# Kernel optimization log

Measured on AMD Instinct MI355X. Metric: run time of the kernel, lower is better.

Reference implementation:

```python
import jax, jax.numpy as jnp
import numpy as np

HID = 1024
NH = 4  # heads for GAT conv1 and all attention blocks
FF = 2048
SLOPE = 0.2


def _ln(x, g, b):
    m = x.mean(-1, keepdims=True)
    v = ((x - m) ** 2).mean(-1, keepdims=True)
    return (x - m) / jnp.sqrt(v + 1e-5) * g + b


def _mha(q, k, v, in_w, in_b, out_w, out_b, nh):
    # q:[B,Lq,E], k/v:[B,Lk,E]; torch MultiheadAttention math (eval mode)
    B, Lq, E = q.shape
    hd = E // nh
    wq, wk, wv = jnp.split(in_w, 3, axis=0)
    bq, bk, bv = jnp.split(in_b, 3)
    qh = (q @ wq.T + bq).reshape(B, Lq, nh, hd)
    kh = (k @ wk.T + bk).reshape(B, -1, nh, hd)
    vh = (v @ wv.T + bv).reshape(B, -1, nh, hd)
    s = jnp.einsum('bqhd,bkhd->bhqk', qh, kh) / jnp.sqrt(jnp.asarray(hd, q.dtype))
    a = jax.nn.softmax(s, axis=-1)
    o = jnp.einsum('bhqk,bkhd->bqhd', a, vh).reshape(B, Lq, E)
    return o @ out_w.T + out_b


def _gatv2(x, edge_index, w_l, b_l, w_r, b_r, att, bias, heads, out_ch):
    # PyG GATv2Conv, flow='target_to_source': i (aggregation dst) = edge_index[0], j = edge_index[1]
    n = x.shape[0]
    dst = edge_index[0]
    src = edge_index[1]
    x_l = (x @ w_l + b_l).reshape(n, heads, out_ch)
    x_r = (x @ w_r + b_r).reshape(n, heads, out_ch)
    msg = x_l[src]                                   # [E,H,C] gathered source features
    e = jax.nn.leaky_relu(msg + x_r[dst], SLOPE)     # [E,H,C]
    alpha = (e * att).sum(-1)                        # [E,H]
    amax = jax.ops.segment_max(alpha, dst, num_segments=n)
    alpha = jnp.exp(alpha - amax[dst])
    denom = jax.ops.segment_sum(alpha, dst, num_segments=n)
    alpha = alpha / (denom[dst] + 1e-16)
    out = jax.ops.segment_sum(msg * alpha[..., None], dst, num_segments=n)
    return out.reshape(n, heads * out_ch) + bias


def setup_inputs() -> dict:
    key = jax.random.key(0)
    ks = iter(jax.random.split(key, 64))
    N, DF, B, L, E_rand = 8000, 768, 32, 14, 96000
    w = lambda *s: jax.random.normal(next(ks), s, jnp.float32) * 0.02
    z = lambda *s: jnp.zeros(s, jnp.float32)
    o = lambda *s: jnp.ones(s, jnp.float32)
    ei = jax.random.randint(next(ks), (2, E_rand), 0, N, jnp.int32)
    self_loops = jnp.tile(jnp.arange(N, dtype=jnp.int32)[None, :], (2, 1))
    inp = {
        'img_feat': jax.random.normal(next(ks), (B, HID), jnp.float32),
        'node_features': jax.random.normal(next(ks), (N, DF), jnp.float32),
        'edge_index': jnp.concatenate([ei, self_loops], axis=1),
        'target_idx': jax.random.randint(next(ks), (L,), 0, N, jnp.int32),
        # GATv2 conv1: 768 -> 4 heads x 256
        'gat1_wl': w(DF, HID), 'gat1_bl': z(HID), 'gat1_wr': w(DF, HID), 'gat1_br': z(HID),
        'gat1_att': w(NH, HID // NH), 'gat1_bias': z(HID),
        # GATv2 conv2: 1024 -> 1 head x 1024
        'gat2_wl': w(HID, HID), 'gat2_bl': z(HID), 'gat2_wr': w(HID, HID), 'gat2_br': z(HID),
        'gat2_att': w(1, HID), 'gat2_bias': z(HID),
        # cross-modal MHA + FFN layer
        'xa_in_w': w(3 * HID, HID), 'xa_in_b': z(3 * HID), 'xa_out_w': w(HID, HID), 'xa_out_b': z(HID),
        'xl_l1_w': w(FF, HID), 'xl_l1_b': z(FF), 'xl_l2_w': w(HID, FF), 'xl_l2_b': z(HID),
        'xl_n1_g': o(HID), 'xl_n1_b': z(HID), 'xl_n2_g': o(HID), 'xl_n2_b': z(HID),
        # 2-layer TransformerEncoder (stacked leading dim = layer)
        'enc_in_w': w(2, 3 * HID, HID), 'enc_in_b': z(2, 3 * HID),
        'enc_out_w': w(2, HID, HID), 'enc_out_b': z(2, HID),
        'enc_l1_w': w(2, FF, HID), 'enc_l1_b': z(2, FF),
        'enc_l2_w': w(2, HID, FF), 'enc_l2_b': z(2, HID),
        'enc_n1_g': o(2, HID), 'enc_n1_b': z(2, HID),
        'enc_n2_g': o(2, HID), 'enc_n2_b': z(2, HID),
        'cls_w': w(1, HID), 'cls_b': z(1),
    }
    return inp


def reference(img_feat, node_features, edge_index, target_idx,
              gat1_wl, gat1_bl, gat1_wr, gat1_br, gat1_att, gat1_bias,
              gat2_wl, gat2_bl, gat2_wr, gat2_br, gat2_att, gat2_bias,
              xa_in_w, xa_in_b, xa_out_w, xa_out_b,
              xl_l1_w, xl_l1_b, xl_l2_w, xl_l2_b, xl_n1_g, xl_n1_b, xl_n2_g, xl_n2_b,
              enc_in_w, enc_in_b, enc_out_w, enc_out_b, enc_l1_w, enc_l1_b, enc_l2_w, enc_l2_b,
              enc_n1_g, enc_n1_b, enc_n2_g, enc_n2_b, cls_w, cls_b):
    x = _gatv2(node_features, edge_index, gat1_wl, gat1_bl, gat1_wr, gat1_br, gat1_att, gat1_bias, NH, HID // NH)
    x = jax.nn.leaky_relu(x, SLOPE)
    x = _gatv2(x, edge_index, gat2_wl, gat2_bl, gat2_wr, gat2_br, gat2_att, gat2_bias, 1, HID)
    t = x[target_idx]                                  # [L, HID]
    B = img_feat.shape[0]
    L = t.shape[0]
    q = jnp.broadcast_to(t[None], (B, L, HID))
    kv = img_feat[:, None, :]                          # [B, 1, HID]
    attn = _mha(q, kv, kv, xa_in_w, xa_in_b, xa_out_w, xa_out_b, NH)
    src = _ln(t[None] + attn, xl_n1_g, xl_n1_b)
    ff = jax.nn.relu(src @ xl_l1_w.T + xl_l1_b) @ xl_l2_w.T + xl_l2_b
    src = _ln(src + ff, xl_n2_g, xl_n2_b)
    for i in range(2):  # TransformerEncoder, post-norm, relu, eval mode
        a = _mha(src, src, src, enc_in_w[i], enc_in_b[i], enc_out_w[i], enc_out_b[i], NH)
        src = _ln(src + a, enc_n1_g[i], enc_n1_b[i])
        f = jax.nn.relu(src @ enc_l1_w[i].T + enc_l1_b[i]) @ enc_l2_w[i].T + enc_l2_b[i]
        src = _ln(src + f, enc_n2_g[i], enc_n2_b[i])
    return (src @ cls_w.T + cls_b)[..., 0]             # [B, L]
```

## Files before the change

### kernel.cpp

```cpp
#include <hip/hip_runtime.h>
#include <hip/hip_bf16.h>

typedef __bf16 bf16;
typedef bf16 bf16x8 __attribute__((ext_vector_type(8)));
typedef bf16 bf16x4 __attribute__((ext_vector_type(4)));
typedef float f32x4 __attribute__((ext_vector_type(4)));

#define HID 1024
#define FFD 2048
#define DEGCAP 1024

typedef __attribute__((address_space(3))) void lds_void;
typedef const __attribute__((address_space(1))) void gm_void;

__device__ __forceinline__ void gload_lds16(const bf16* g, bf16* l)
{
    __builtin_amdgcn_global_load_lds((gm_void*)g, (lds_void*)l, 16, 0, 0);
}

__global__ __launch_bounds__(256) void cvt_bf16_kernel(
    const float* __restrict__ src, bf16* __restrict__ dst, long n)
{
    long i = ((long)blockIdx.x * 256 + threadIdx.x) * 4;
    if (i >= n) return;
    float4 f = *(const float4*)&src[i];
    bf16x4 v = {(bf16)f.x, (bf16)f.y, (bf16)f.z, (bf16)f.w};
    *(bf16x4*)&dst[i] = v;
}

__global__ __launch_bounds__(256) void cvt_t_bf16_kernel(
    const float* __restrict__ in, bf16* __restrict__ out, int R, int C)
{
    __shared__ bf16 tile[32][33];
    const int c0 = blockIdx.x * 32, r0 = blockIdx.y * 32;
    const int tx = threadIdx.x & 31, ty = threadIdx.x >> 5;
#pragma unroll
    for (int i = ty; i < 32; i += 8)
        tile[i][tx] = (bf16)in[(long)(r0 + i) * C + c0 + tx];
    __syncthreads();
#pragma unroll
    for (int i = ty; i < 32; i += 8)
        out[(long)(c0 + i) * R + r0 + tx] = tile[tx][i];
}

template <int ACT, int OUTBF16>
__global__ __launch_bounds__(256) void gemm_bf16_kernel(
    const bf16* __restrict__ A, const bf16* __restrict__ B,
    const float* __restrict__ bias, void* __restrict__ Cp,
    int M, int N, int K)
{
    const int tid  = threadIdx.x;
    const int bn   = blockIdx.x, bm = blockIdx.y;
    const int lane = tid & 63, wave = tid >> 6;
    const int wr   = wave >> 1, wc = wave & 1;

    __shared__ bf16 As[128][32];
    __shared__ bf16 Bs[128][32];

    f32x4 acc[4][4] = {};

    const int srow = wave * 16 + (lane >> 2);
    const int scol = (lane & 3) << 3;
    const long ga0 = (long)min(bm * 128 + srow,      M - 1) * K + scol;
    const long ga1 = (long)min(bm * 128 + srow + 64, M - 1) * K + scol;
    const long gb0 = (long)(bn * 128 + srow)      * K + scol;
    const long gb1 = (long)(bn * 128 + srow + 64) * K + scol;
    bf16* ldsA0 = &As[0][0] + wave * 512;
    bf16* ldsA1 = &As[0][0] + 2048 + wave * 512;
    bf16* ldsB0 = &Bs[0][0] + wave * 512;
    bf16* ldsB1 = &Bs[0][0] + 2048 + wave * 512;

    const int quad = lane >> 4;
    const int mr   = lane & 15;
    const int kf   = quad * 8;

    for (int k0 = 0; k0 < K; k0 += 32) {
        gload_lds16(A + ga0 + k0, ldsA0);
        gload_lds16(A + ga1 + k0, ldsA1);
        gload_lds16(B + gb0 + k0, ldsB0);
        gload_lds16(B + gb1 + k0, ldsB1);
        __syncthreads();

        bf16x8 af[4], bfr[4];
#pragma unroll
        for (int i = 0; i < 4; ++i) af[i]  = *(const bf16x8*)&As[wr * 64 + i * 16 + mr][kf];
#pragma unroll
        for (int j = 0; j < 4; ++j) bfr[j] = *(const bf16x8*)&Bs[wc * 64 + j * 16 + mr][kf];
#pragma unroll
        for (int i = 0; i < 4; ++i)
#pragma unroll
            for (int j = 0; j < 4; ++j)
                acc[i][j] = __builtin_amdgcn_mfma_f32_16x16x32_bf16(af[i], bfr[j], acc[i][j], 0, 0, 0);
        __syncthreads();
    }

    const int crow = quad * 4;
#pragma unroll
    for (int i = 0; i < 4; ++i) {
#pragma unroll
        for (int j = 0; j < 4; ++j) {
            const int   col = bn * 128 + wc * 64 + j * 16 + mr;
            const float bv  = bias[col];
#pragma unroll
            for (int r = 0; r < 4; ++r) {
                const int row = bm * 128 + wr * 64 + i * 16 + crow + r;
                if (row < M) {
                    float v = acc[i][j][r] + bv;
                    if (ACT == 1) v = fmaxf(v, 0.f);
                    if (OUTBF16) ((bf16*)Cp)[(long)row * N + col] = (bf16)v;
                    else         ((float*)Cp)[(long)row * N + col] = v;
                }
            }
        }
    }
}

template <int KS>
__global__ __launch_bounds__(256) void gemm_sk_kernel(
    const float* __restrict__ A, const float* __restrict__ Bt,
    float* __restrict__ part, int M, int N, int K)
{
    const int tid  = threadIdx.x;
    const int bn   = blockIdx.x, bm = blockIdx.y, kz = blockIdx.z;
    const int lane = tid & 63, wave = tid >> 6;
    const int wr   = wave >> 1, wc = wave & 1;

    __shared__ bf16 As[128][40];
    __shared__ bf16 Bs[128][40];

    f32x4 acc[4][4] = {};

    const int  lr = tid >> 2;
    const int  lc = (tid & 3) << 3;
    const long a0 = (long)min(bm * 128 + lr,      M - 1) * K;
    const long a1 = (long)min(bm * 128 + lr + 64, M - 1) * K;
    const long b0 = (long)(bn * 128 + lr)      * K;
    const long b1 = (long)(bn * 128 + lr + 64) * K;

    const int quad = lane >> 4;
    const int mr   = lane & 15;
    const int kf   = quad * 8;

    const int Kc   = K / KS;
    const int kbeg = kz * Kc, kend = kbeg + Kc;

    float4 ra[4], rb[4];
    auto load_chunk = [&](int k0) {
        ra[0] = *(const float4*)&A[a0 + k0 + lc];
        ra[1] = *(const float4*)&A[a0 + k0 + lc + 4];
        ra[2] = *(const float4*)&A[a1 + k0 + lc];
        ra[3] = *(const float4*)&A[a1 + k0 + lc + 4];
        rb[0] = *(const float4*)&Bt[b0 + k0 + lc];
        rb[1] = *(const float4*)&Bt[b0 + k0 + lc + 4];
        rb[2] = *(const float4*)&Bt[b1 + k0 + lc];
        rb[3] = *(const float4*)&Bt[b1 + k0 + lc + 4];
    };

    load_chunk(kbeg);
    for (int k0 = kbeg; k0 < kend; k0 += 32) {
        {
            bf16x8 v0 = {(bf16)ra[0].x,(bf16)ra[0].y,(bf16)ra[0].z,(bf16)ra[0].w,
                         (bf16)ra[1].x,(bf16)ra[1].y,(bf16)ra[1].z,(bf16)ra[1].w};
            *(bf16x8*)&As[lr][lc] = v0;
            bf16x8 v1 = {(bf16)ra[2].x,(bf16)ra[2].y,(bf16)ra[2].z,(bf16)ra[2].w,
                         (bf16)ra[3].x,(bf16)ra[3].y,(bf16)ra[3].z,(bf16)ra[3].w};
            *(bf16x8*)&As[lr + 64][lc] = v1;
            bf16x8 v2 = {(bf16)rb[0].x,(bf16)rb[0].y,(bf16)rb[0].z,(bf16)rb[0].w,
                         (bf16)rb[1].x,(bf16)rb[1].y,(bf16)rb[1].z,(bf16)rb[1].w};
            *(bf16x8*)&Bs[lr][lc] = v2;
            bf16x8 v3 = {(bf16)rb[2].x,(bf16)rb[2].y,(bf16)rb[2].z,(bf16)rb[2].w,
                         (bf16)rb[3].x,(bf16)rb[3].y,(bf16)rb[3].z,(bf16)rb[3].w};
            *(bf16x8*)&Bs[lr + 64][lc] = v3;
        }
        __syncthreads();
        if (k0 + 32 < kend) load_chunk(k0 + 32);

        bf16x8 af[4], bfr[4];
#pragma unroll
        for (int i = 0; i < 4; ++i) af[i]  = *(const bf16x8*)&As[wr * 64 + i * 16 + mr][kf];
#pragma unroll
        for (int j = 0; j < 4; ++j) bfr[j] = *(const bf16x8*)&Bs[wc * 64 + j * 16 + mr][kf];
#pragma unroll
        for (int i = 0; i < 4; ++i)
#pragma unroll
            for (int j = 0; j < 4; ++j)
                acc[i][j] = __builtin_amdgcn_mfma_f32_16x16x32_bf16(af[i], bfr[j], acc[i][j], 0, 0, 0);
        __syncthreads();
    }

    const int crow = quad * 4;
    float* dst = part + (size_t)kz * M * N;
#pragma unroll
    for (int i = 0; i < 4; ++i) {
#pragma unroll
        for (int j = 0; j < 4; ++j) {
            const int col = bn * 128 + wc * 64 + j * 16 + mr;
#pragma unroll
            for (int r = 0; r < 4; ++r) {
                const int row = bm * 128 + wr * 64 + i * 16 + crow + r;
                if (row < M) dst[(long)row * N + col] = acc[i][j][r];
            }
        }
    }
}

template <int ACT, int KS>
__global__ __launch_bounds__(256) void sk_reduce_kernel(
    const float* __restrict__ part, const float* __restrict__ bias,
    float* __restrict__ C, long MN, int N)
{
    long i = ((long)blockIdx.x * 256 + threadIdx.x) * 4;
    if (i >= MN) return;
    float4 s = *(const float4*)&part[i];
#pragma unroll
    for (int k = 1; k < KS; ++k) {
        float4 p = *(const float4*)&part[(size_t)k * MN + i];
        s.x += p.x; s.y += p.y; s.z += p.z; s.w += p.w;
    }
    const int col = (int)(i % N);
    float4 bv = *(const float4*)&bias[col];
    s.x += bv.x; s.y += bv.y; s.z += bv.z; s.w += bv.w;
    if (ACT) {
        s.x = fmaxf(s.x, 0.f); s.y = fmaxf(s.y, 0.f);
        s.z = fmaxf(s.z, 0.f); s.w = fmaxf(s.w, 0.f);
    }
    *(float4*)&C[i] = s;
}

__global__ void zero_i32_kernel(int* __restrict__ p, int n)
{
    int i = blockIdx.x * 256 + threadIdx.x;
    if (i < n) p[i] = 0;
}

__global__ void hist_kernel(const int* __restrict__ ei, int E, int* __restrict__ deg)
{
    int e = blockIdx.x * 256 + threadIdx.x;
    if (e < E) atomicAdd(&deg[ei[e]], 1);
}

__global__ void scan_kernel(const int* __restrict__ deg, int* __restrict__ rowstart,
                            int* __restrict__ cursor, int n)
{
    __shared__ int sm[1024];
    __shared__ int carry;
    if (threadIdx.x == 0) carry = 0;
    __syncthreads();
    for (int base = 0; base < n; base += 1024) {
        int i = base + threadIdx.x;
        int v = (i < n) ? deg[i] : 0;
        sm[threadIdx.x] = v;
        __syncthreads();
        for (int off = 1; off < 1024; off <<= 1) {
            int t = (threadIdx.x >= off) ? sm[threadIdx.x - off] : 0;
            __syncthreads();
            sm[threadIdx.x] += t;
            __syncthreads();
        }
        if (i < n) { int ex = carry + sm[threadIdx.x] - v; rowstart[i] = ex; cursor[i] = ex; }
        __syncthreads();
        if (threadIdx.x == 0) carry += sm[1023];
        __syncthreads();
    }
    if (threadIdx.x == 0) rowstart[n] = carry;
}

__global__ void scatter_kernel(const int* __restrict__ ei, int E,
                               int* __restrict__ cursor, int* __restrict__ eidx)
{
    int e = blockIdx.x * 256 + threadIdx.x;
    if (e < E) { int p = atomicAdd(&cursor[ei[e]], 1); eidx[p] = e; }
}

template <int NH, int LRELU, int OUTBF16>
__global__ __launch_bounds__(256) void gat_fused_kernel(
    const bf16* __restrict__ xl, const bf16* __restrict__ xr,
    const float* __restrict__ att,
    const int* __restrict__ ei, const int* __restrict__ rowstart,
    const int* __restrict__ eidx, const float* __restrict__ bias,
    void* __restrict__ outp, int E)
{
    const int n = blockIdx.x;
    const int tid = threadIdx.x, lane = tid & 63, wave = tid >> 6;
    const int rs = rowstart[n];
    int deg = rowstart[n + 1] - rs;
    if (deg > DEGCAP) deg = DEGCAP;

    __shared__ bf16  xr_sm[HID];
    __shared__ int   src_sm[DEGCAP];
    __shared__ float alpha_sm[DEGCAP * NH];

    {
        const int c0 = tid * 4;
        *(bf16x4*)&xr_sm[c0] = *(const bf16x4*)&xr[(long)n * HID + c0];
    }
    for (int j = tid; j < deg; j += 256)
        src_sm[j] = ei[E + eidx[rs + j]];
    __syncthreads();

    for (int j = wave; j < deg; j += 4) {
        const int s = src_sm[j];
        const int c0 = lane * 16;
        bf16x8 a0 = *(const bf16x8*)&xl[(long)s * HID + c0];
        bf16x8 a1 = *(const bf16x8*)&xl[(long)s * HID + c0 + 8];
        bf16x8 b0 = *(const bf16x8*)&xr_sm[c0];
        bf16x8 b1 = *(const bf16x8*)&xr_sm[c0 + 8];
        float4 t0 = *(const float4*)&att[c0];
        float4 t1 = *(const float4*)&att[c0 + 4];
        float4 t2 = *(const float4*)&att[c0 + 8];
        float4 t3 = *(const float4*)&att[c0 + 12];
        const float* at = (const float*)&t0;
        float av[16] = {t0.x,t0.y,t0.z,t0.w, t1.x,t1.y,t1.z,t1.w,
                        t2.x,t2.y,t2.z,t2.w, t3.x,t3.y,t3.z,t3.w};
        (void)at;
        float acc = 0.f;
#pragma unroll
        for (int t = 0; t < 8; ++t) {
            float v = (float)a0[t] + (float)b0[t];
            v = v > 0.f ? v : 0.2f * v;
            acc += v * av[t];
            float w = (float)a1[t] + (float)b1[t];
            w = w > 0.f ? w : 0.2f * w;
            acc += w * av[8 + t];
        }
        if (NH == 4) {
#pragma unroll
            for (int o = 1; o < 16; o <<= 1) acc += __shfl_xor(acc, o);
            if ((lane & 15) == 0) alpha_sm[j * NH + (lane >> 4)] = acc;
        } else {
#pragma unroll
            for (int o = 1; o < 64; o <<= 1) acc += __shfl_xor(acc, o);
            if (lane == 0) alpha_sm[j] = acc;
        }
    }
    __syncthreads();

    if (wave < NH) {
        float m = -1e30f;
        for (int j = lane; j < deg; j += 64) m = fmaxf(m, alpha_sm[j * NH + wave]);
        for (int o = 32; o; o >>= 1) m = fmaxf(m, __shfl_down(m, o));
        m = __shfl(m, 0);
        float s = 0.f;
        for (int j = lane; j < deg; j += 64) s += expf(alpha_sm[j * NH + wave] - m);
        for (int o = 32; o; o >>= 1) s += __shfl_down(s, o);
        s = __shfl(s, 0);
        const float dinv = 1.f / (s + 1e-16f);
        for (int j = lane; j < deg; j += 64)
            alpha_sm[j * NH + wave] = expf(alpha_sm[j * NH + wave] - m) * dinv;
    }
    __syncthreads();

    const int c0 = tid * 4;
    const int hh = (NH == 4) ? (tid >> 6) : 0;
    float a0 = 0, a1 = 0, a2 = 0, a3 = 0;
    for (int j = 0; j < deg; ++j) {
        const float alpha = alpha_sm[j * NH + hh];
        bf16x4 mv = *(const bf16x4*)&xl[(long)src_sm[j] * HID + c0];
        a0 += alpha * (float)mv[0]; a1 += alpha * (float)mv[1];
        a2 += alpha * (float)mv[2]; a3 += alpha * (float)mv[3];
    }
    float o4[4] = {a0, a1, a2, a3};
#pragma unroll
    for (int k = 0; k < 4; ++k) {
        float v = o4[k] + bias[c0 + k];
        if (LRELU) v = v > 0.f ? v : 0.2f * v;
        if (OUTBF16) ((bf16*)outp)[(long)n * HID + c0 + k] = (bf16)v;
        else         ((float*)outp)[(long)n * HID + c0 + k] = v;
    }
}

__device__ __forceinline__ void ln_finish(float v[4], int c0, const float* g,
                                          const float* beta, float* outrow)
{
    float s1 = v[0] + v[1] + v[2] + v[3];
    float s2 = v[0] * v[0] + v[1] * v[1] + v[2] * v[2] + v[3] * v[3];
    __shared__ float red[8];
    for (int o = 32; o; o >>= 1) { s1 += __shfl_down(s1, o); s2 += __shfl_down(s2, o); }
    const int wave = threadIdx.x >> 6, lane = threadIdx.x & 63;
    if (lane == 0) { red[wave] = s1; red[4 + wave] = s2; }
    __syncthreads();
    if (threadIdx.x == 0) {
        red[0] += red[1] + red[2] + red[3];
        red[4] += red[5] + red[6] + red[7];
    }
    __syncthreads();
    const float mean = red[0] * (1.f / HID);
    const float var  = fmaxf(red[4] * (1.f / HID) - mean * mean, 0.f);
    const float rstd = rsqrtf(var + 1e-5f);
#pragma unroll
    for (int k = 0; k < 4; ++k) {
        int c = c0 + k;
        outrow[c] = (v[k] - mean) * rstd * g[c] + beta[c];
    }
}

__global__ __launch_bounds__(256) void ln_cross_kernel(
    const float* __restrict__ x2, const int* __restrict__ tidx,
    const float* __restrict__ attnb, const float* __restrict__ g,
    const float* __restrict__ beta, float* __restrict__ out, int L)
{
    const int row = blockIdx.x;
    const int b = row / L, l = row - b * L;
    const long tr = (long)tidx[l] * HID, ar = (long)b * HID;
    const int c0 = threadIdx.x * 4;
    float v[4];
#pragma unroll
    for (int k = 0; k < 4; ++k)
        v[k] = x2[tr + c0 + k] + attnb[ar + c0 + k];
    ln_finish(v, c0, g, beta, out + (long)row * HID);
}

__global__ __launch_bounds__(256) void ln_res_kernel(
    float* __restrict__ srcio, const float* __restrict__ delta,
    const float* __restrict__ g, const float* __restrict__ beta)
{
    const long row = blockIdx.x;
    const int c0 = threadIdx.x * 4;
    float v[4];
#pragma unroll
    for (int k = 0; k < 4; ++k)
        v[k] = srcio[row * HID + c0 + k] + delta[row * HID + c0 + k];
    ln_finish(v, c0, g, beta, srcio + row * HID);
}

__global__ __launch_bounds__(256) void self_attn_kernel(
    const float* __restrict__ qkv, float* __restrict__ out, int L)
{
    const int b = blockIdx.x >> 2, h = blockIdx.x & 3;
    const int tid = threadIdx.x;
    __shared__ float q[16][256], kk[16][256], vv[16][256];
    __shared__ float sc[16][16];
    for (int i = tid; i < L * 256; i += 256) {
        const int l = i >> 8, d = i & 255;
        const long rb = (long)(b * L + l) * 3072 + h * 256 + d;
        q[l][d]  = qkv[rb];
        kk[l][d] = qkv[rb + 1024];
        vv[l][d] = qkv[rb + 2048];
    }
    __syncthreads();
    if (tid < L * L) {
        const int l1 = tid / L, l2 = tid - l1 * L;
        float s = 0.f;
        for (int d = 0; d < 256; ++d) s += q[l1][d] * kk[l2][d];
        sc[l1][l2] = s * 0.0625f;
    }
    __syncthreads();
    if (tid < L) {
        float mx = -1e30f;
        for (int j = 0; j < L; ++j) mx = fmaxf(mx, sc[tid][j]);
        float ssum = 0.f;
        for (int j = 0; j < L; ++j) { float e = expf(sc[tid][j] - mx); sc[tid][j] = e; ssum += e; }
        const float inv = 1.f / ssum;
        for (int j = 0; j < L; ++j) sc[tid][j] *= inv;
    }
    __syncthreads();
    for (int l1 = 0; l1 < L; ++l1) {
        float a = 0.f;
        for (int l2 = 0; l2 < L; ++l2) a += sc[l1][l2] * vv[l2][tid];
        out[(long)(b * L + l1) * HID + h * 256 + tid] = a;
    }
}

__global__ __launch_bounds__(256) void cls_kernel(
    const float* __restrict__ src, const float* __restrict__ w,
    const float* __restrict__ b, float* __restrict__ out, int rows)
{
    const int row = blockIdx.x * 4 + (threadIdx.x >> 6);
    const int lane = threadIdx.x & 63;
    if (row >= rows) return;
    float s = 0.f;
    for (int c = lane; c < HID; c += 64) s += src[(long)row * HID + c] * w[c];
    for (int o = 32; o; o >>= 1) s += __shfl_down(s, o);
    if (lane == 0) out[row] = s + b[0];
}

extern "C" void kernel_launch(void* const* d_in, const int* in_sizes, int n_in,
                              void* d_out, int out_size, void* d_ws, size_t ws_size,
                              hipStream_t stream)
{
    const float* img_feat      = (const float*)d_in[0];
    const float* node_features = (const float*)d_in[1];
    const int*   edge_index    = (const int*)d_in[2];
    const int*   target_idx    = (const int*)d_in[3];
    const float* gat1_wl  = (const float*)d_in[4];
    const float* gat1_bl  = (const float*)d_in[5];
    const float* gat1_wr  = (const float*)d_in[6];
    const float* gat1_br  = (const float*)d_in[7];
    const float* gat1_att = (const float*)d_in[8];
    const float* gat1_bias= (const float*)d_in[9];
    const float* gat2_wl  = (const float*)d_in[10];
    const float* gat2_bl  = (const float*)d_in[11];
    const float* gat2_wr  = (const float*)d_in[12];
    const float* gat2_br  = (const float*)d_in[13];
    const float* gat2_att = (const float*)d_in[14];
    const float* gat2_bias= (const float*)d_in[15];
    const float* xa_in_w  = (const float*)d_in[16];
    const float* xa_in_b  = (const float*)d_in[17];
    const float* xa_out_w = (const float*)d_in[18];
    const float* xa_out_b = (const float*)d_in[19];
    const float* xl_l1_w  = (const float*)d_in[20];
    const float* xl_l1_b  = (const float*)d_in[21];
    const float* xl_l2_w  = (const float*)d_in[22];
    const float* xl_l2_b  = (const float*)d_in[23];
    const float* xl_n1_g  = (const float*)d_in[24];
    const float* xl_n1_b  = (const float*)d_in[25];
    const float* xl_n2_g  = (const float*)d_in[26];
    const float* xl_n2_b  = (const float*)d_in[27];
    const float* enc_in_w = (const float*)d_in[28];
    const float* enc_in_b = (const float*)d_in[29];
    const float* enc_out_w= (const float*)d_in[30];
    const float* enc_out_b= (const float*)d_in[31];
    const float* enc_l1_w = (const float*)d_in[32];
    const float* enc_l1_b = (const float*)d_in[33];
    const float* enc_l2_w = (const float*)d_in[34];
    const float* enc_l2_b = (const float*)d_in[35];
    const float* enc_n1_g = (const float*)d_in[36];
    const float* enc_n1_b = (const float*)d_in[37];
    const float* enc_n2_g = (const float*)d_in[38];
    const float* enc_n2_b = (const float*)d_in[39];
    const float* cls_w    = (const float*)d_in[40];
    const float* cls_b    = (const float*)d_in[41];

    const int DF = in_sizes[4] / HID;
    const int Nn = in_sizes[1] / DF;
    const int E  = in_sizes[2] / 2;
    const int L  = in_sizes[3];
    const int B  = in_sizes[0] / HID;
    const int R  = B * L;

    char* basep = (char*)d_ws;
    size_t off = 0;
    auto alloc = [&](size_t bytes) -> char* {
        char* r = basep + off; off += (bytes + 255) & ~(size_t)255; return r;
    };
    size_t regA_need = 0;
    {
        auto sz = [&](size_t b) { regA_need += (b + 255) & ~(size_t)255; };
        sz((size_t)Nn * DF * 2); sz((size_t)DF * HID * 2); sz((size_t)DF * HID * 2);
        sz((size_t)HID * HID * 2); sz((size_t)HID * HID * 2); sz((size_t)Nn * HID * 2);
    }
    size_t regA_bytes = regA_need > (size_t)Nn * HID * 4 ? regA_need : (size_t)Nn * HID * 4;
    char* regionA = alloc(regA_bytes);
    {
        size_t aoff = 0;
        auto allocA = [&](size_t bytes) -> char* {
            char* r = regionA + aoff; aoff += (bytes + 255) & ~(size_t)255; return r;
        };
        bf16* nfb  = (bf16*)allocA((size_t)Nn * DF * 2);
        bf16* w1lT = (bf16*)allocA((size_t)DF * HID * 2);
        bf16* w1rT = (bf16*)allocA((size_t)DF * HID * 2);
        bf16* w2lT = (bf16*)allocA((size_t)HID * HID * 2);
        bf16* w2rT = (bf16*)allocA((size_t)HID * HID * 2);
        bf16* x1   = (bf16*)allocA((size_t)Nn * HID * 2);

        float* x2  = (float*)regionA;

        bf16* xlb = (bf16*)alloc((size_t)Nn * HID * 2);
        bf16* xrb = (bf16*)alloc((size_t)Nn * HID * 2);
        int*   deg      = (int*)alloc((size_t)Nn * 4);
        int*   rowstart = (int*)alloc((size_t)(Nn + 1) * 4);
        int*   cursor   = (int*)alloc((size_t)(Nn + 1) * 4);
        int*   eidx     = (int*)alloc((size_t)E * 4);
        float* skpart   = (float*)alloc((size_t)4 * R * 3 * HID * 4);

        char* qb = (char*)xlb; size_t qoff = 0;
        auto alloc2 = [&](size_t bytes) -> char* {
            char* r = qb + qoff; qoff += (bytes + 255) & ~(size_t)255; return r;
        };
        float* vproj  = (float*)alloc2((size_t)B * HID * 4);
        float* attnb  = (float*)alloc2((size_t)B * HID * 4);
        float* srcbuf = (float*)alloc2((size_t)R * HID * 4);
        float* h1buf  = (float*)alloc2((size_t)R * FFD * 4);
        float* ffbuf  = (float*)alloc2((size_t)R * HID * 4);
        float* qkvbuf = (float*)alloc2((size_t)R * 3 * HID * 4);
        float* aoutbuf= (float*)alloc2((size_t)R * HID * 4);

        const int gE  = (E + 255) / 256;
        const int gMn = (Nn + 127) / 128;

        auto gemm_sk4 = [&](const float* A, const float* Bt, const float* bias,
                            float* C, int M, int N, int K, int act) {
            gemm_sk_kernel<4><<<dim3(N / 128, (M + 127) / 128, 4), 256, 0, stream>>>(
                A, Bt, skpart, M, N, K);
            long MN = (long)M * N;
            int g = (int)((MN / 4 + 255) / 256);
            if (act) sk_reduce_kernel<1,4><<<g, 256, 0, stream>>>(skpart, bias, C, MN, N);
            else     sk_reduce_kernel<0,4><<<g, 256, 0, stream>>>(skpart, bias, C, MN, N);
        };
        auto gemm_sk8 = [&](const float* A, const float* Bt, const float* bias,
                            float* C, int M, int N, int K, int act) {
            gemm_sk_kernel<8><<<dim3(N / 128, (M + 127) / 128, 8), 256, 0, stream>>>(
                A, Bt, skpart, M, N, K);
            long MN = (long)M * N;
            int g = (int)((MN / 4 + 255) / 256);
            if (act) sk_reduce_kernel<1,8><<<g, 256, 0, stream>>>(skpart, bias, C, MN, N);
            else     sk_reduce_kernel<0,8><<<g, 256, 0, stream>>>(skpart, bias, C, MN, N);
        };

        zero_i32_kernel<<<(Nn + 255) / 256, 256, 0, stream>>>(deg, Nn);
        hist_kernel<<<gE, 256, 0, stream>>>(edge_index, E, deg);
        scan_kernel<<<1, 1024, 0, stream>>>(deg, rowstart, cursor, Nn);
        scatter_kernel<<<gE, 256, 0, stream>>>(edge_index, E, cursor, eidx);

        cvt_bf16_kernel<<<(int)(((long)Nn * DF / 4 + 255) / 256), 256, 0, stream>>>(
            node_features, nfb, (long)Nn * DF);
        cvt_t_bf16_kernel<<<dim3(HID / 32, DF / 32), 256, 0, stream>>>(gat1_wl, w1lT, DF, HID);
        cvt_t_bf16_kernel<<<dim3(HID / 32, DF / 32), 256, 0, stream>>>(gat1_wr, w1rT, DF, HID);
        cvt_t_bf16_kernel<<<dim3(HID / 32, HID / 32), 256, 0, stream>>>(gat2_wl, w2lT, HID, HID);
        cvt_t_bf16_kernel<<<dim3(HID / 32, HID / 32), 256, 0, stream>>>(gat2_wr, w2rT, HID, HID);

        gemm_bf16_kernel<0,1><<<dim3(HID / 128, gMn), 256, 0, stream>>>(nfb, w1lT, gat1_bl, xlb, Nn, HID, DF);
        gemm_bf16_kernel<0,1><<<dim3(HID / 128, gMn), 256, 0, stream>>>(nfb, w1rT, gat1_br, xrb, Nn, HID, DF);
        gat_fused_kernel<4,1,1><<<Nn, 256, 0, stream>>>(xlb, xrb, gat1_att, edge_index,
                                                        rowstart, eidx, gat1_bias, x1, E);

        gemm_bf16_kernel<0,1><<<dim3(HID / 128, gMn), 256, 0, stream>>>(x1, w2lT, gat2_bl, xlb, Nn, HID, HID);
        gemm_bf16_kernel<0,1><<<dim3(HID / 128, gMn), 256, 0, stream>>>(x1, w2rT, gat2_br, xrb, Nn, HID, HID);
        gat_fused_kernel<1,0,0><<<Nn, 256, 0, stream>>>(xlb, xrb, gat2_att, edge_index,
                                                        rowstart, eidx, gat2_bias, x2, E);

        gemm_sk8(img_feat, xa_in_w + (size_t)2 * HID * HID, xa_in_b + 2 * HID, vproj, B, HID, HID, 0);
        gemm_sk8(vproj, xa_out_w, xa_out_b, attnb, B, HID, HID, 0);
        ln_cross_kernel<<<R, 256, 0, stream>>>(x2, target_idx, attnb, xl_n1_g, xl_n1_b, srcbuf, L);

        gemm_sk4(srcbuf, xl_l1_w, xl_l1_b, h1buf, R, FFD, HID, 1);
        gemm_sk8(h1buf, xl_l2_w, xl_l2_b, ffbuf, R, HID, FFD, 0);
        ln_res_kernel<<<R, 256, 0, stream>>>(srcbuf, ffbuf, xl_n2_g, xl_n2_b);

        for (int i = 0; i < 2; ++i) {
            gemm_sk4(srcbuf, enc_in_w + (size_t)i * 3 * HID * HID, enc_in_b + i * 3 * HID,
                     qkvbuf, R, 3 * HID, HID, 0);
            self_attn_kernel<<<B * 4, 256, 0, stream>>>(qkvbuf, ffbuf, L);
            gemm_sk8(ffbuf, enc_out_w + (size_t)i * HID * HID, enc_out_b + i * HID,
                     aoutbuf, R, HID, HID, 0);
            ln_res_kernel<<<R, 256, 0, stream>>>(srcbuf, aoutbuf, enc_n1_g + i * HID, enc_n1_b + i * HID);
            gemm_sk4(srcbuf, enc_l1_w + (size_t)i * FFD * HID, enc_l1_b + i * FFD,
                     h1buf, R, FFD, HID, 1);
            gemm_sk8(h1buf, enc_l2_w + (size_t)i * HID * FFD, enc_l2_b + i * HID,
                     ffbuf, R, HID, FFD, 0);
            ln_res_kernel<<<R, 256, 0, stream>>>(srcbuf, ffbuf, enc_n2_g + i * HID, enc_n2_b + i * HID);
        }

        cls_kernel<<<(R + 3) / 4, 256, 0, stream>>>(srcbuf, cls_w, cls_b, (float*)d_out, R);
    }
}
```

Before: 737.2 us.

## Fuse split-K reduce with residual LayerNorm, cache GAT rows, swizzle GEMM blocks

```diff
diff --git a/kernel.cpp b/kernel.cpp
--- a/kernel.cpp
+++ b/kernel.cpp
@@ -8,7 +8,8 @@
 
 #define HID 1024
 #define FFD 2048
-#define DEGCAP 1024
+#define DEGCAP 256
+#define ROWCAP 16
 
 typedef __attribute__((address_space(3))) void lds_void;
 typedef const __attribute__((address_space(1))) void gm_void;
@@ -47,10 +48,14 @@
 __global__ __launch_bounds__(256) void gemm_bf16_kernel(
     const bf16* __restrict__ A, const bf16* __restrict__ B,
     const float* __restrict__ bias, void* __restrict__ Cp,
-    int M, int N, int K)
-{
+    int M, int N, int K, int NB)
+{
+    const int total = gridDim.x;
+    const int h = blockIdx.x;
+    const int t = (total % 8 == 0) ? ((h & 7) * (total >> 3) + (h >> 3)) : h;
+    const int bn = t % NB, bm = t / NB;
+
     const int tid  = threadIdx.x;
-    const int bn   = blockIdx.x, bm = blockIdx.y;
     const int lane = tid & 63, wave = tid >> 6;
     const int wr   = wave >> 1, wc = wave & 1;
 
@@ -227,6 +232,53 @@
     *(float4*)&C[i] = s;
 }
 
+__device__ __forceinline__ void ln_finish(float v[4], int c0, const float* g,
+                                          const float* beta, float* outrow)
+{
+    float s1 = v[0] + v[1] + v[2] + v[3];
+    float s2 = v[0] * v[0] + v[1] * v[1] + v[2] * v[2] + v[3] * v[3];
+    __shared__ float red[8];
+    for (int o = 32; o; o >>= 1) { s1 += __shfl_down(s1, o); s2 += __shfl_down(s2, o); }
+    const int wave = threadIdx.x >> 6, lane = threadIdx.x & 63;
+    if (lane == 0) { red[wave] = s1; red[4 + wave] = s2; }
+    __syncthreads();
+    if (threadIdx.x == 0) {
+        red[0] += red[1] + red[2] + red[3];
+        red[4] += red[5] + red[6] + red[7];
+    }
+    __syncthreads();
+    const float mean = red[0] * (1.f / HID);
+    const float var  = fmaxf(red[4] * (1.f / HID) - mean * mean, 0.f);
+    const float rstd = rsqrtf(var + 1e-5f);
+#pragma unroll
+    for (int k = 0; k < 4; ++k) {
+        int c = c0 + k;
+        outrow[c] = (v[k] - mean) * rstd * g[c] + beta[c];
+    }
+}
+
+template <int KS>
+__global__ __launch_bounds__(256) void sk_reduce_ln_kernel(
+    const float* __restrict__ part, const float* __restrict__ bias,
+    float* __restrict__ srcio, const float* __restrict__ g,
+    const float* __restrict__ beta, long MN)
+{
+    const long row = blockIdx.x;
+    const int c0 = threadIdx.x * 4;
+    const long base = row * HID + c0;
+    float4 s = *(const float4*)&part[base];
+#pragma unroll
+    for (int k = 1; k < KS; ++k) {
+        float4 p = *(const float4*)&part[(size_t)k * MN + base];
+        s.x += p.x; s.y += p.y; s.z += p.z; s.w += p.w;
+    }
+    float4 bv = *(const float4*)&bias[c0];
+    float4 rv = *(const float4*)&srcio[base];
+    float v[4] = {s.x + bv.x + rv.x, s.y + bv.y + rv.y,
+                  s.z + bv.z + rv.z, s.w + bv.w + rv.w};
+    ln_finish(v, c0, g, beta, srcio + row * HID);
+}
+
 __global__ void zero_i32_kernel(int* __restrict__ p, int n)
 {
     int i = blockIdx.x * 256 + threadIdx.x;
@@ -287,8 +339,9 @@
     if (deg > DEGCAP) deg = DEGCAP;
 
     __shared__ bf16  xr_sm[HID];
+    __shared__ bf16  rows_sm[ROWCAP][HID];
     __shared__ int   src_sm[DEGCAP];
-    __shared__ float alpha_sm[DEGCAP * NH];
+    __shared__ float logit_sm[DEGCAP * NH];
 
     {
         const int c0 = tid * 4;
@@ -298,63 +351,75 @@
         src_sm[j] = ei[E + eidx[rs + j]];
     __syncthreads();
 
+    const int cA = lane * 8, cB = 512 + lane * 8;
     for (int j = wave; j < deg; j += 4) {
-        const int s = src_sm[j];
-        const int c0 = lane * 16;
-        bf16x8 a0 = *(const bf16x8*)&xl[(long)s * HID + c0];
-        bf16x8 a1 = *(const bf16x8*)&xl[(long)s * HID + c0 + 8];
-        bf16x8 b0 = *(const bf16x8*)&xr_sm[c0];
-        bf16x8 b1 = *(const bf16x8*)&xr_sm[c0 + 8];
-        float4 t0 = *(const float4*)&att[c0];
-        float4 t1 = *(const float4*)&att[c0 + 4];
-        float4 t2 = *(const float4*)&att[c0 + 8];
-        float4 t3 = *(const float4*)&att[c0 + 12];
-        const float* at = (const float*)&t0;
-        float av[16] = {t0.x,t0.y,t0.z,t0.w, t1.x,t1.y,t1.z,t1.w,
-                        t2.x,t2.y,t2.z,t2.w, t3.x,t3.y,t3.z,t3.w};
-        (void)at;
-        float acc = 0.f;
+        const long base = (long)src_sm[j] * HID;
+        bf16x8 a0 = *(const bf16x8*)&xl[base + cA];
+        bf16x8 a1 = *(const bf16x8*)&xl[base + cB];
+        if (j < ROWCAP) {
+            *(bf16x8*)&rows_sm[j][cA] = a0;
+            *(bf16x8*)&rows_sm[j][cB] = a1;
+        }
+        bf16x8 b0 = *(const bf16x8*)&xr_sm[cA];
+        bf16x8 b1 = *(const bf16x8*)&xr_sm[cB];
+        float4 tA0 = *(const float4*)&att[cA], tA1 = *(const float4*)&att[cA + 4];
+        float4 tB0 = *(const float4*)&att[cB], tB1 = *(const float4*)&att[cB + 4];
+        float avA[8] = {tA0.x,tA0.y,tA0.z,tA0.w, tA1.x,tA1.y,tA1.z,tA1.w};
+        float avB[8] = {tB0.x,tB0.y,tB0.z,tB0.w, tB1.x,tB1.y,tB1.z,tB1.w};
+        float accA = 0.f, accB = 0.f;
 #pragma unroll
         for (int t = 0; t < 8; ++t) {
             float v = (float)a0[t] + (float)b0[t];
             v = v > 0.f ? v : 0.2f * v;
-            acc += v * av[t];
+            accA += v * avA[t];
             float w = (float)a1[t] + (float)b1[t];
             w = w > 0.f ? w : 0.2f * w;
-            acc += w * av[8 + t];
+            accB += w * avB[t];
         }
         if (NH == 4) {
 #pragma unroll
-            for (int o = 1; o < 16; o <<= 1) acc += __shfl_xor(acc, o);
-            if ((lane & 15) == 0) alpha_sm[j * NH + (lane >> 4)] = acc;
+            for (int o = 1; o < 32; o <<= 1) {
+                accA += __shfl_xor(accA, o);
+                accB += __shfl_xor(accB, o);
+            }
+            if (lane == 0)  { logit_sm[j * 4 + 0] = accA; logit_sm[j * 4 + 2] = accB; }
+            if (lane == 32) { logit_sm[j * 4 + 1] = accA; logit_sm[j * 4 + 3] = accB; }
         } else {
-#pragma unroll
-            for (int o = 1; o < 64; o <<= 1) acc += __shfl_xor(acc, o);
-            if (lane == 0) alpha_sm[j] = acc;
+            float s = accA + accB;
+#pragma unroll
+            for (int o = 1; o < 64; o <<= 1) s += __shfl_xor(s, o);
+            if (lane == 0) logit_sm[j] = s;
         }
     }
     __syncthreads();
 
     if (wave < NH) {
         float m = -1e30f;
-        for (int j = lane; j < deg; j += 64) m = fmaxf(m, alpha_sm[j * NH + wave]);
+        for (int j = lane; j < deg; j += 64) m = fmaxf(m, logit_sm[j * NH + wave]);
         for (int o = 32; o; o >>= 1) m = fmaxf(m, __shfl_down(m, o));
         m = __shfl(m, 0);
         float s = 0.f;
-        for (int j = lane; j < deg; j += 64) s += expf(alpha_sm[j * NH + wave] - m);
+        for (int j = lane; j < deg; j += 64) s += expf(logit_sm[j * NH + wave] - m);
         for (int o = 32; o; o >>= 1) s += __shfl_down(s, o);
         s = __shfl(s, 0);
         const float dinv = 1.f / (s + 1e-16f);
         for (int j = lane; j < deg; j += 64)
-            alpha_sm[j * NH + wave] = expf(alpha_sm[j * NH + wave] - m) * dinv;
+            logit_sm[j * NH + wave] = expf(logit_sm[j * NH + wave] - m) * dinv;
     }
     __syncthreads();
 
     const int c0 = tid * 4;
     const int hh = (NH == 4) ? (tid >> 6) : 0;
     float a0 = 0, a1 = 0, a2 = 0, a3 = 0;
-    for (int j = 0; j < deg; ++j) {
-        const float alpha = alpha_sm[j * NH + hh];
+    const int dlds = deg < ROWCAP ? deg : ROWCAP;
+    for (int j = 0; j < dlds; ++j) {
+        const float alpha = logit_sm[j * NH + hh];
+        bf16x4 mv = *(const bf16x4*)&rows_sm[j][c0];
+        a0 += alpha * (float)mv[0]; a1 += alpha * (float)mv[1];
+        a2 += alpha * (float)mv[2]; a3 += alpha * (float)mv[3];
+    }
+    for (int j = ROWCAP; j < deg; ++j) {
+        const float alpha = logit_sm[j * NH + hh];
         bf16x4 mv = *(const bf16x4*)&xl[(long)src_sm[j] * HID + c0];
         a0 += alpha * (float)mv[0]; a1 += alpha * (float)mv[1];
         a2 += alpha * (float)mv[2]; a3 += alpha * (float)mv[3];
@@ -369,31 +434,6 @@
     }
 }
 
-__device__ __forceinline__ void ln_finish(float v[4], int c0, const float* g,
-                                          const float* beta, float* outrow)
-{
-    float s1 = v[0] + v[1] + v[2] + v[3];
-    float s2 = v[0] * v[0] + v[1] * v[1] + v[2] * v[2] + v[3] * v[3];
-    __shared__ float red[8];
-    for (int o = 32; o; o >>= 1) { s1 += __shfl_down(s1, o); s2 += __shfl_down(s2, o); }
-    const int wave = threadIdx.x >> 6, lane = threadIdx.x & 63;
-    if (lane == 0) { red[wave] = s1; red[4 + wave] = s2; }
-    __syncthreads();
-    if (threadIdx.x == 0) {
-        red[0] += red[1] + red[2] + red[3];
-        red[4] += red[5] + red[6] + red[7];
-    }
-    __syncthreads();
-    const float mean = red[0] * (1.f / HID);
-    const float var  = fmaxf(red[4] * (1.f / HID) - mean * mean, 0.f);
-    const float rstd = rsqrtf(var + 1e-5f);
-#pragma unroll
-    for (int k = 0; k < 4; ++k) {
-        int c = c0 + k;
-        outrow[c] = (v[k] - mean) * rstd * g[c] + beta[c];
-    }
-}
-
 __global__ __launch_bounds__(256) void ln_cross_kernel(
     const float* __restrict__ x2, const int* __restrict__ tidx,
     const float* __restrict__ attnb, const float* __restrict__ g,
@@ -408,19 +448,6 @@
     for (int k = 0; k < 4; ++k)
         v[k] = x2[tr + c0 + k] + attnb[ar + c0 + k];
     ln_finish(v, c0, g, beta, out + (long)row * HID);
-}
-
-__global__ __launch_bounds__(256) void ln_res_kernel(
-    float* __restrict__ srcio, const float* __restrict__ delta,
-    const float* __restrict__ g, const float* __restrict__ beta)
-{
-    const long row = blockIdx.x;
-    const int c0 = threadIdx.x * 4;
-    float v[4];
-#pragma unroll
-    for (int k = 0; k < 4; ++k)
-        v[k] = srcio[row * HID + c0 + k] + delta[row * HID + c0 + k];
-    ln_finish(v, c0, g, beta, srcio + row * HID);
 }
 
 __global__ __launch_bounds__(256) void self_attn_kernel(
@@ -561,7 +588,7 @@
         int*   rowstart = (int*)alloc((size_t)(Nn + 1) * 4);
         int*   cursor   = (int*)alloc((size_t)(Nn + 1) * 4);
         int*   eidx     = (int*)alloc((size_t)E * 4);
-        float* skpart   = (float*)alloc((size_t)4 * R * 3 * HID * 4);
+        float* skpart   = (float*)alloc((size_t)8 * R * 3 * HID * 4);
 
         char* qb = (char*)xlb; size_t qoff = 0;
         auto alloc2 = [&](size_t bytes) -> char* {
@@ -573,10 +600,10 @@
         float* h1buf  = (float*)alloc2((size_t)R * FFD * 4);
         float* ffbuf  = (float*)alloc2((size_t)R * HID * 4);
         float* qkvbuf = (float*)alloc2((size_t)R * 3 * HID * 4);
-        float* aoutbuf= (float*)alloc2((size_t)R * HID * 4);
 
         const int gE  = (E + 255) / 256;
         const int gMn = (Nn + 127) / 128;
+        const long MNr = (long)R * HID;
 
         auto gemm_sk4 = [&](const float* A, const float* Bt, const float* bias,
                             float* C, int M, int N, int K, int act) {
@@ -596,6 +623,12 @@
             if (act) sk_reduce_kernel<1,8><<<g, 256, 0, stream>>>(skpart, bias, C, MN, N);
             else     sk_reduce_kernel<0,8><<<g, 256, 0, stream>>>(skpart, bias, C, MN, N);
         };
+        auto gemm_sk8_ln = [&](const float* A, const float* Bt, const float* bias,
+                               float* srcio, const float* g, const float* beta, int K) {
+            gemm_sk_kernel<8><<<dim3(HID / 128, (R + 127) / 128, 8), 256, 0, stream>>>(
+                A, Bt, skpart, R, HID, K);
+            sk_reduce_ln_kernel<8><<<R, 256, 0, stream>>>(skpart, bias, srcio, g, beta, MNr);
+        };
 
         zero_i32_kernel<<<(Nn + 255) / 256, 256, 0, stream>>>(deg, Nn);
         hist_kernel<<<gE, 256, 0, stream>>>(edge_index, E, deg);
@@ -609,13 +642,13 @@
         cvt_t_bf16_kernel<<<dim3(HID / 32, HID / 32), 256, 0, stream>>>(gat2_wl, w2lT, HID, HID);
         cvt_t_bf16_kernel<<<dim3(HID / 32, HID / 32), 256, 0, stream>>>(gat2_wr, w2rT, HID, HID);
 
-        gemm_bf16_kernel<0,1><<<dim3(HID / 128, gMn), 256, 0, stream>>>(nfb, w1lT, gat1_bl, xlb, Nn, HID, DF);
-        gemm_bf16_kernel<0,1><<<dim3(HID / 128, gMn), 256, 0, stream>>>(nfb, w1rT, gat1_br, xrb, Nn, HID, DF);
+        gemm_bf16_kernel<0,1><<<8 * gMn, 256, 0, stream>>>(nfb, w1lT, gat1_bl, xlb, Nn, HID, DF, 8);
+        gemm_bf16_kernel<0,1><<<8 * gMn, 256, 0, stream>>>(nfb, w1rT, gat1_br, xrb, Nn, HID, DF, 8);
         gat_fused_kernel<4,1,1><<<Nn, 256, 0, stream>>>(xlb, xrb, gat1_att, edge_index,
                                                         rowstart, eidx, gat1_bias, x1, E);
 
-        gemm_bf16_kernel<0,1><<<dim3(HID / 128, gMn), 256, 0, stream>>>(x1, w2lT, gat2_bl, xlb, Nn, HID, HID);
-        gemm_bf16_kernel<0,1><<<dim3(HID / 128, gMn), 256, 0, stream>>>(x1, w2rT, gat2_br, xrb, Nn, HID, HID);
+        gemm_bf16_kernel<0,1><<<8 * gMn, 256, 0, stream>>>(x1, w2lT, gat2_bl, xlb, Nn, HID, HID, 8);
+        gemm_bf16_kernel<0,1><<<8 * gMn, 256, 0, stream>>>(x1, w2rT, gat2_br, xrb, Nn, HID, HID, 8);
         gat_fused_kernel<1,0,0><<<Nn, 256, 0, stream>>>(xlb, xrb, gat2_att, edge_index,
                                                         rowstart, eidx, gat2_bias, x2, E);
 
@@ -624,21 +657,18 @@
         ln_cross_kernel<<<R, 256, 0, stream>>>(x2, target_idx, attnb, xl_n1_g, xl_n1_b, srcbuf, L);
 
         gemm_sk4(srcbuf, xl_l1_w, xl_l1_b, h1buf, R, FFD, HID, 1);
-        gemm_sk8(h1buf, xl_l2_w, xl_l2_b, ffbuf, R, HID, FFD, 0);
-        ln_res_kernel<<<R, 256, 0, stream>>>(srcbuf, ffbuf, xl_n2_g, xl_n2_b);
+        gemm_sk8_ln(h1buf, xl_l2_w, xl_l2_b, srcbuf, xl_n2_g, xl_n2_b, FFD);
 
         for (int i = 0; i < 2; ++i) {
             gemm_sk4(srcbuf, enc_in_w + (size_t)i * 3 * HID * HID, enc_in_b + i * 3 * HID,
                      qkvbuf, R, 3 * HID, HID, 0);
             self_attn_kernel<<<B * 4, 256, 0, stream>>>(qkvbuf, ffbuf, L);
-            gemm_sk8(ffbuf, enc_out_w + (size_t)i * HID * HID, enc_out_b + i * HID,
-                     aoutbuf, R, HID, HID, 0);
-            ln_res_kernel<<<R, 256, 0, stream>>>(srcbuf, aoutbuf, enc_n1_g + i * HID, enc_n1_b + i * HID);
+            gemm_sk8_ln(ffbuf, enc_out_w + (size_t)i * HID * HID, enc_out_b + i * HID,
+                        srcbuf, enc_n1_g + i * HID, enc_n1_b + i * HID, HID);
             gemm_sk4(srcbuf, enc_l1_w + (size_t)i * FFD * HID, enc_l1_b + i * FFD,
                      h1buf, R, FFD, HID, 1);
-            gemm_sk8(h1buf, enc_l2_w + (size_t)i * HID * FFD, enc_l2_b + i * HID,
-                     ffbuf, R, HID, FFD, 0);
-            ln_res_kernel<<<R, 256, 0, stream>>>(srcbuf, ffbuf, enc_n2_g + i * HID, enc_n2_b + i * HID);
+            gemm_sk8_ln(h1buf, enc_l2_w + (size_t)i * HID * FFD, enc_l2_b + i * HID,
+                        srcbuf, enc_n2_g + i * HID, enc_n2_b + i * HID, FFD);
         }
 
         cls_kernel<<<(R + 3) / 4, 256, 0, stream>>>(srcbuf, cls_w, cls_b, (float*)d_out, R);
```

Result: no change. 724.6 us (-1.7%).
